# Optimization experiments

Hardware: AMD Instinct MI355X
Metric: run time of the kernel (lower is better)

Reference implementation:

```python
import jax, jax.numpy as jnp
import numpy as np

HID = 256
IN_DIM = 64
OUT_DIM = 4
B = 2048
T = 128


def setup_inputs() -> dict:
    key = jax.random.key(0)
    ks = jax.random.split(key, 12)
    s = lambda k, shp, fan: jax.random.normal(k, shp, jnp.float32) / np.sqrt(fan)
    return {
        "static_input": jax.random.normal(ks[0], (B, IN_DIM), jnp.float32),
        "times": jnp.arange(T, dtype=jnp.float32) * 0.05,  # increasing grid
        "W_in": s(ks[1], (IN_DIM, HID), IN_DIM), "b_in": jnp.zeros((HID,), jnp.float32),
        "W1": s(ks[2], (HID, HID), HID), "b1": jnp.zeros((HID,), jnp.float32),
        "W2": s(ks[3], (HID, HID), HID), "b2": jnp.zeros((HID,), jnp.float32),
        "W_pk": s(ks[4], (HID, OUT_DIM), HID), "b_pk": jnp.zeros((OUT_DIM,), jnp.float32),
        "W_pd": s(ks[5], (HID, 1), HID), "b_pd": jnp.zeros((1,), jnp.float32),
    }


def _odefunc(h, W1, b1, W2, b2):
    # Linear -> Tanh -> Linear (autonomous: ignores t, as in the torch ODEFunc)
    return jnp.tanh(h @ W1 + b1) @ W2 + b2


def reference(static_input, times, W_in, b_in, W1, b1, W2, b2, W_pk, b_pk, W_pd, b_pd):
    h0 = static_input @ W_in + b_in  # [B, H]
    f = lambda h: _odefunc(h, W1, b1, W2, b2)
    dts = times[1:] - times[:-1]  # [T-1]

    def rk4_step(h, dt):
        k1 = f(h)
        k2 = f(h + 0.5 * dt * k1)
        k3 = f(h + 0.5 * dt * k2)
        k4 = f(h + dt * k3)
        h_next = h + (dt / 6.0) * (k1 + 2.0 * k2 + 2.0 * k3 + k4)
        return h_next, h_next

    _, h_rest = jax.lax.scan(rk4_step, h0, dts)  # [T-1, B, H]
    h_ts = jnp.concatenate([h0[None], h_rest], axis=0)  # [T, B, H]
    h_ts = jnp.transpose(h_ts, (1, 0, 2))  # [B, T, H]
    pk_pred = h_ts @ W_pk + b_pk          # [B, T, OUT_DIM]
    pd_pred = h_ts[:, -1, :] @ W_pd + b_pd  # [B, 1]
    return (pk_pred, pd_pred)
```

## Files before the change

### kernel.cpp

```cpp
#include <hip/hip_runtime.h>
#include <hip/hip_bf16.h>
#include <stdint.h>

#define H       256
#define INDIM   64
#define TSTEPS  128
#define BATCH   2048
#define MROWS   8
#define OUTD    4

typedef __attribute__((ext_vector_type(8))) short bf16x8;
typedef __attribute__((ext_vector_type(4))) float f32x4;

__device__ __forceinline__ short b2s(float x) {
  __hip_bfloat16 h = __float2bfloat16(x);
  return __builtin_bit_cast(short, h);
}

__device__ __forceinline__ int swz(int m, int n) {
  return (m * H + n) ^ ((m & 7) << 3);
}

__device__ __forceinline__ float swap_hilo(float a, float b) {
#if __has_builtin(__builtin_amdgcn_permlane32_swap)
  typedef unsigned int u32x2 __attribute__((ext_vector_type(2)));
  u32x2 r = __builtin_amdgcn_permlane32_swap(
      __builtin_bit_cast(unsigned int, a),
      __builtin_bit_cast(unsigned int, b), false, false);
  return __builtin_bit_cast(float, r[0]);
#else
  float t = __shfl_xor(b, 32);
  return (threadIdx.x & 32) ? t : a;
#endif
}

__global__ __launch_bounds__(512, 1) void node_kernel(
    const float* __restrict__ g_static, const float* __restrict__ g_times,
    const float* __restrict__ g_Win, const float* __restrict__ g_bin,
    const float* __restrict__ g_W1, const float* __restrict__ g_b1,
    const float* __restrict__ g_W2, const float* __restrict__ g_b2,
    const float* __restrict__ g_Wpk, const float* __restrict__ g_bpk,
    const float* __restrict__ g_Wpd, const float* __restrict__ g_bpd,
    float* __restrict__ g_out)
{
  __shared__ __align__(16) short arg_lds[MROWS * H];
  __shared__ __align__(16) short h1_lds[MROWS * H];
  __shared__ __align__(16) short wpk_lds[8 * 64 * 8];
  __shared__ float h_lds[MROWS * H];
  __shared__ float s_lds[MROWS * INDIM];
  __shared__ float t_lds[TSTEPS];

  const int tid   = threadIdx.x;
  const int lane  = tid & 63;
  const int wid   = tid >> 6;
  const int g     = lane >> 4;
  const int c     = lane & 15;
  const int b0    = blockIdx.x * MROWS;
  const int ncol0 = wid * 32;
  const int am    = lane & 7;
  const int gg    = (lane >> 4) & 1;
  const int hh    = lane >> 5;
  const int colu  = ncol0 + 16 * hh + c;
  const int dm    = 4 * g;

  if (tid < TSTEPS) t_lds[tid] = g_times[tid];

  const float b1u2 = 2.0f * g_b1[colu];
  const float b2u  = g_b2[colu];
  const float bpkc = g_bpk[c & 3];
  const float bpdv = g_bpd[0];
  float wpd[4];
#pragma unroll
  for (int j = 0; j < 4; ++j) wpd[j] = g_Wpd[lane + 64 * j];

  int ra[8], wa[4], ha[4];
#pragma unroll
  for (int kt = 0; kt < 8; ++kt) ra[kt] = swz(am, kt * 32 + g * 8);
#pragma unroll
  for (int r = 0; r < 4; ++r) {
    wa[r] = swz(4 * gg + r, colu);
    ha[r] = (4 * gg + r) * H + colu;
  }

  bf16x8 w1f[8][2], w2f[8][2];
#pragma unroll
  for (int kt = 0; kt < 8; ++kt) {
#pragma unroll
    for (int nt = 0; nt < 2; ++nt) {
      const int n  = ncol0 + nt * 16 + c;
      const int kb = kt * 32 + g * 8;
      bf16x8 f1, f2;
#pragma unroll
      for (int u = 0; u < 8; ++u) {
        f1[u] = b2s(g_W1[(kb + u) * H + n]);
        f2[u] = b2s(g_W2[(kb + u) * H + n]);
      }
      w1f[kt][nt] = f1;
      w2f[kt][nt] = f2;
    }
  }

  if (wid == 0) {
#pragma unroll
    for (int kt = 0; kt < 8; ++kt) {
      bf16x8 f;
#pragma unroll
      for (int u = 0; u < 8; ++u) {
        const int k = kt * 32 + g * 8 + u;
        f[u] = (c < OUTD) ? b2s(g_Wpk[k * OUTD + c]) : (short)0;
      }
      *(bf16x8*)(wpk_lds + kt * 512 + lane * 8) = f;
    }
  }

  s_lds[tid] = g_static[(b0 + (tid >> 6)) * INDIM + (tid & 63)];
  __syncthreads();
  {
    const int m  = tid >> 6;
    const int n0 = (tid & 63) * 4;
    float a0 = g_bin[n0], a1 = g_bin[n0 + 1], a2 = g_bin[n0 + 2], a3 = g_bin[n0 + 3];
#pragma unroll 8
    for (int k = 0; k < INDIM; ++k) {
      const float sv = s_lds[m * INDIM + k];
      const f32x4 w = *(const f32x4*)(g_Win + k * H + n0);
      a0 += sv * w[0]; a1 += sv * w[1]; a2 += sv * w[2]; a3 += sv * w[3];
    }
    h_lds[m * H + n0] = a0;     h_lds[m * H + n0 + 1] = a1;
    h_lds[m * H + n0 + 2] = a2; h_lds[m * H + n0 + 3] = a3;
    arg_lds[swz(m, n0)]     = b2s(a0);
    arg_lds[swz(m, n0 + 1)] = b2s(a1);
    arg_lds[swz(m, n0 + 2)] = b2s(a2);
    arg_lds[swz(m, n0 + 3)] = b2s(a3);
  }
  __syncthreads();

  float hb[4];
#pragma unroll
  for (int r = 0; r < 4; ++r) hb[r] = h_lds[ha[r]];

  auto emit_pk = [&](int t) {
    if (wid == 0) {
      f32x4 acc = {0.f, 0.f, 0.f, 0.f};
#pragma unroll
      for (int kt = 0; kt < 8; ++kt) {
        const bf16x8 aA = *(const bf16x8*)(arg_lds + ra[kt]);
        const bf16x8 bW = *(const bf16x8*)(wpk_lds + kt * 512 + lane * 8);
        acc = __builtin_amdgcn_mfma_f32_16x16x32_bf16(aA, bW, acc, 0, 0, 0);
      }
      if (g < 2 && c < OUTD) {
#pragma unroll
        for (int r = 0; r < 4; ++r)
          g_out[((size_t)(b0 + dm + r) * TSTEPS + t) * OUTD + c] = acc[r] + bpkc;
      }
    }
  };

  emit_pk(0);

  for (int t = 1; t < TSTEPS; ++t) {
    const float dt = t_lds[t] - t_lds[t - 1];
    const float s6 = dt * (1.0f / 6.0f);
    float ks[4];

#pragma unroll
    for (int ev = 0; ev < 4; ++ev) {
      f32x4 A0 = {0.f,0.f,0.f,0.f}, A1 = {0.f,0.f,0.f,0.f};
      f32x4 B0 = {0.f,0.f,0.f,0.f}, B1 = {0.f,0.f,0.f,0.f};
#pragma unroll
      for (int kt = 0; kt < 4; ++kt) {
        const bf16x8 aA = *(const bf16x8*)(arg_lds + ra[kt]);
        const bf16x8 aB = *(const bf16x8*)(arg_lds + ra[kt + 4]);
        A0 = __builtin_amdgcn_mfma_f32_16x16x32_bf16(aA, w1f[kt][0], A0, 0, 0, 0);
        A1 = __builtin_amdgcn_mfma_f32_16x16x32_bf16(aA, w1f[kt][1], A1, 0, 0, 0);
        B0 = __builtin_amdgcn_mfma_f32_16x16x32_bf16(aB, w1f[kt + 4][0], B0, 0, 0, 0);
        B1 = __builtin_amdgcn_mfma_f32_16x16x32_bf16(aB, w1f[kt + 4][1], B1, 0, 0, 0);
      }
#pragma unroll
      for (int r = 0; r < 4; ++r) {
        const float v = swap_hilo(A0[r] + B0[r], A1[r] + B1[r]);
        const float e = __expf(__builtin_fmaf(2.0f, v, b1u2));
        const float th = 1.0f - __fdividef(2.0f, e + 1.0f);
        h1_lds[wa[r]] = b2s(th);
      }
      __syncthreads();

      A0 = f32x4{0.f,0.f,0.f,0.f}; A1 = f32x4{0.f,0.f,0.f,0.f};
      B0 = f32x4{0.f,0.f,0.f,0.f}; B1 = f32x4{0.f,0.f,0.f,0.f};
#pragma unroll
      for (int kt = 0; kt < 4; ++kt) {
        const bf16x8 aA = *(const bf16x8*)(h1_lds + ra[kt]);
        const bf16x8 aB = *(const bf16x8*)(h1_lds + ra[kt + 4]);
        A0 = __builtin_amdgcn_mfma_f32_16x16x32_bf16(aA, w2f[kt][0], A0, 0, 0, 0);
        A1 = __builtin_amdgcn_mfma_f32_16x16x32_bf16(aA, w2f[kt][1], A1, 0, 0, 0);
        B0 = __builtin_amdgcn_mfma_f32_16x16x32_bf16(aB, w2f[kt + 4][0], B0, 0, 0, 0);
        B1 = __builtin_amdgcn_mfma_f32_16x16x32_bf16(aB, w2f[kt + 4][1], B1, 0, 0, 0);
      }
#pragma unroll
      for (int r = 0; r < 4; ++r) {
        const float kv = swap_hilo(A0[r] + B0[r], A1[r] + B1[r]) + b2u;
        if (ev == 0)      ks[r] = kv;
        else if (ev == 3) ks[r] += kv;
        else              ks[r] += 2.0f * kv;
        if (ev < 3) {
          const float cc = (ev == 2) ? dt : 0.5f * dt;
          arg_lds[wa[r]] = b2s(__builtin_fmaf(cc, kv, hb[r]));
        } else {
          hb[r] = __builtin_fmaf(s6, ks[r], hb[r]);
          arg_lds[wa[r]] = b2s(hb[r]);
        }
      }
      __syncthreads();
    }
    emit_pk(t);
  }

#pragma unroll
  for (int r = 0; r < 4; ++r) h_lds[ha[r]] = hb[r];
  __syncthreads();
  {
    float p = 0.0f;
#pragma unroll
    for (int j = 0; j < 4; ++j) p += h_lds[wid * H + lane + 64 * j] * wpd[j];
#pragma unroll
    for (int m = 1; m < 64; m <<= 1) p += __shfl_xor(p, m);
    if (lane == 0) g_out[(size_t)BATCH * TSTEPS * OUTD + b0 + wid] = p + bpdv;
  }
}

extern "C" void kernel_launch(void* const* d_in, const int* in_sizes, int n_in,
                              void* d_out, int out_size, void* d_ws, size_t ws_size,
                              hipStream_t stream) {
  const float* g_static = (const float*)d_in[0];
  const float* g_times  = (const float*)d_in[1];
  const float* g_Win    = (const float*)d_in[2];
  const float* g_bin    = (const float*)d_in[3];
  const float* g_W1     = (const float*)d_in[4];
  const float* g_b1     = (const float*)d_in[5];
  const float* g_W2     = (const float*)d_in[6];
  const float* g_b2     = (const float*)d_in[7];
  const float* g_Wpk    = (const float*)d_in[8];
  const float* g_bpk    = (const float*)d_in[9];
  const float* g_Wpd    = (const float*)d_in[10];
  const float* g_bpd    = (const float*)d_in[11];

  node_kernel<<<dim3(BATCH / MROWS), dim3(512), 0, stream>>>(
      g_static, g_times, g_Win, g_bin, g_W1, g_b1, g_W2, g_b2,
      g_Wpk, g_bpk, g_Wpd, g_bpd, (float*)d_out);
}
```

Before: 660.7 us.

## Use 16-row batch tiles with 16 waves each owning 16 columns

Doubles the batch rows per block to 16 so each MFMA's 16 M-rows are all real work instead of half padding, and doubles threads to 1024 so each wave owns 16 hidden columns. Each wave's weight fragment register footprint halves and the permlane swap merge step goes away. The grid halves to 128 blocks, and every sync now involves 16 waves, which may hurt latency across the sequential RK4 chain. The Wpk LDS layout is also remapped so all 16 output rows come out correctly.

```diff
diff --git a/kernel.cpp b/kernel.cpp
--- a/kernel.cpp
+++ b/kernel.cpp
@@ -6,7 +6,7 @@
 #define INDIM   64
 #define TSTEPS  128
 #define BATCH   2048
-#define MROWS   8
+#define MROWS   16
 #define OUTD    4
 
 typedef __attribute__((ext_vector_type(8))) short bf16x8;
@@ -17,24 +17,17 @@
   return __builtin_bit_cast(short, h);
 }
 
-__device__ __forceinline__ int swz(int m, int n) {
-  return (m * H + n) ^ ((m & 7) << 3);
-}
-
-__device__ __forceinline__ float swap_hilo(float a, float b) {
-#if __has_builtin(__builtin_amdgcn_permlane32_swap)
-  typedef unsigned int u32x2 __attribute__((ext_vector_type(2)));
-  u32x2 r = __builtin_amdgcn_permlane32_swap(
-      __builtin_bit_cast(unsigned int, a),
-      __builtin_bit_cast(unsigned int, b), false, false);
-  return __builtin_bit_cast(float, r[0]);
-#else
-  float t = __shfl_xor(b, 32);
-  return (threadIdx.x & 32) ? t : a;
-#endif
-}
-
-__global__ __launch_bounds__(512, 1) void node_kernel(
+__device__ __forceinline__ int sidx(int m, int n) {
+  return m * H + (n ^ ((m & 7) << 3));
+}
+__device__ __forceinline__ int wpk_slot(int lane) {
+  return (((lane & 3) << 1) | ((lane >> 4) & 1)) |
+         (((lane >> 2) & 3) << 3) | (((lane >> 5) & 1) << 5);
+}
+
+#define MFMA(a, b, c) __builtin_amdgcn_mfma_f32_16x16x32_bf16((a), (b), (c), 0, 0, 0)
+
+__global__ __launch_bounds__(1024, 4) void node_kernel(
     const float* __restrict__ g_static, const float* __restrict__ g_times,
     const float* __restrict__ g_Win, const float* __restrict__ g_bin,
     const float* __restrict__ g_W1, const float* __restrict__ g_b1,
@@ -53,15 +46,12 @@
   const int tid   = threadIdx.x;
   const int lane  = tid & 63;
   const int wid   = tid >> 6;
-  const int g     = lane >> 4;
+  const int q     = lane >> 4;
   const int c     = lane & 15;
   const int b0    = blockIdx.x * MROWS;
-  const int ncol0 = wid * 32;
-  const int am    = lane & 7;
-  const int gg    = (lane >> 4) & 1;
-  const int hh    = lane >> 5;
-  const int colu  = ncol0 + 16 * hh + c;
-  const int dm    = 4 * g;
+  const int ncol0 = wid * 16;
+  const int arow  = lane & 15;
+  const int colu  = ncol0 + c;
 
   if (tid < TSTEPS) t_lds[tid] = g_times[tid];
 
@@ -75,49 +65,46 @@
 
   int ra[8], wa[4], ha[4];
 #pragma unroll
-  for (int kt = 0; kt < 8; ++kt) ra[kt] = swz(am, kt * 32 + g * 8);
+  for (int kt = 0; kt < 8; ++kt) ra[kt] = sidx(arow, kt * 32 + q * 8);
 #pragma unroll
   for (int r = 0; r < 4; ++r) {
-    wa[r] = swz(4 * gg + r, colu);
-    ha[r] = (4 * gg + r) * H + colu;
-  }
-
-  bf16x8 w1f[8][2], w2f[8][2];
+    wa[r] = sidx(4 * q + r, colu);
+    ha[r] = (4 * q + r) * H + colu;
+  }
+
+  bf16x8 w1f[8], w2f[8];
 #pragma unroll
   for (int kt = 0; kt < 8; ++kt) {
-#pragma unroll
-    for (int nt = 0; nt < 2; ++nt) {
-      const int n  = ncol0 + nt * 16 + c;
-      const int kb = kt * 32 + g * 8;
-      bf16x8 f1, f2;
-#pragma unroll
-      for (int u = 0; u < 8; ++u) {
-        f1[u] = b2s(g_W1[(kb + u) * H + n]);
-        f2[u] = b2s(g_W2[(kb + u) * H + n]);
-      }
-      w1f[kt][nt] = f1;
-      w2f[kt][nt] = f2;
-    }
+    const int kb = kt * 32 + q * 8;
+    bf16x8 f1, f2;
+#pragma unroll
+    for (int u = 0; u < 8; ++u) {
+      f1[u] = b2s(g_W1[(kb + u) * H + colu]);
+      f2[u] = b2s(g_W2[(kb + u) * H + colu]);
+    }
+    w1f[kt] = f1;
+    w2f[kt] = f2;
   }
 
   if (wid == 0) {
+    const int slot = wpk_slot(lane);
 #pragma unroll
     for (int kt = 0; kt < 8; ++kt) {
       bf16x8 f;
 #pragma unroll
       for (int u = 0; u < 8; ++u) {
-        const int k = kt * 32 + g * 8 + u;
+        const int k = kt * 32 + q * 8 + u;
         f[u] = (c < OUTD) ? b2s(g_Wpk[k * OUTD + c]) : (short)0;
       }
-      *(bf16x8*)(wpk_lds + kt * 512 + lane * 8) = f;
-    }
-  }
-
-  s_lds[tid] = g_static[(b0 + (tid >> 6)) * INDIM + (tid & 63)];
+      *(bf16x8*)(wpk_lds + kt * 512 + slot * 8) = f;
+    }
+  }
+
+  s_lds[tid] = g_static[(b0 + wid) * INDIM + lane];
   __syncthreads();
   {
-    const int m  = tid >> 6;
-    const int n0 = (tid & 63) * 4;
+    const int m  = wid;
+    const int n0 = lane * 4;
     float a0 = g_bin[n0], a1 = g_bin[n0 + 1], a2 = g_bin[n0 + 2], a3 = g_bin[n0 + 3];
 #pragma unroll 8
     for (int k = 0; k < INDIM; ++k) {
@@ -127,10 +114,10 @@
     }
     h_lds[m * H + n0] = a0;     h_lds[m * H + n0 + 1] = a1;
     h_lds[m * H + n0 + 2] = a2; h_lds[m * H + n0 + 3] = a3;
-    arg_lds[swz(m, n0)]     = b2s(a0);
-    arg_lds[swz(m, n0 + 1)] = b2s(a1);
-    arg_lds[swz(m, n0 + 2)] = b2s(a2);
-    arg_lds[swz(m, n0 + 3)] = b2s(a3);
+    arg_lds[sidx(m, n0)]     = b2s(a0);
+    arg_lds[sidx(m, n0 + 1)] = b2s(a1);
+    arg_lds[sidx(m, n0 + 2)] = b2s(a2);
+    arg_lds[sidx(m, n0 + 3)] = b2s(a3);
   }
   __syncthreads();
 
@@ -138,25 +125,27 @@
 #pragma unroll
   for (int r = 0; r < 4; ++r) hb[r] = h_lds[ha[r]];
 
+  const int wslot = wpk_slot(lane);
   auto emit_pk = [&](int t) {
     if (wid == 0) {
       f32x4 acc = {0.f, 0.f, 0.f, 0.f};
 #pragma unroll
       for (int kt = 0; kt < 8; ++kt) {
         const bf16x8 aA = *(const bf16x8*)(arg_lds + ra[kt]);
-        const bf16x8 bW = *(const bf16x8*)(wpk_lds + kt * 512 + lane * 8);
-        acc = __builtin_amdgcn_mfma_f32_16x16x32_bf16(aA, bW, acc, 0, 0, 0);
-      }
-      if (g < 2 && c < OUTD) {
+        const bf16x8 bW = *(const bf16x8*)(wpk_lds + kt * 512 + wslot * 8);
+        acc = MFMA(aA, bW, acc);
+      }
+      if (c < OUTD) {
 #pragma unroll
         for (int r = 0; r < 4; ++r)
-          g_out[((size_t)(b0 + dm + r) * TSTEPS + t) * OUTD + c] = acc[r] + bpkc;
+          g_out[((size_t)(b0 + 4 * q + r) * TSTEPS + t) * OUTD + c] = acc[r] + bpkc;
       }
     }
   };
 
   emit_pk(0);
 
+  const f32x4 vz = {0.f, 0.f, 0.f, 0.f};
   for (int t = 1; t < TSTEPS; ++t) {
     const float dt = t_lds[t] - t_lds[t - 1];
     const float s6 = dt * (1.0f / 6.0f);
@@ -164,49 +153,47 @@
 
 #pragma unroll
     for (int ev = 0; ev < 4; ++ev) {
-      f32x4 A0 = {0.f,0.f,0.f,0.f}, A1 = {0.f,0.f,0.f,0.f};
-      f32x4 B0 = {0.f,0.f,0.f,0.f}, B1 = {0.f,0.f,0.f,0.f};
-#pragma unroll
-      for (int kt = 0; kt < 4; ++kt) {
-        const bf16x8 aA = *(const bf16x8*)(arg_lds + ra[kt]);
-        const bf16x8 aB = *(const bf16x8*)(arg_lds + ra[kt + 4]);
-        A0 = __builtin_amdgcn_mfma_f32_16x16x32_bf16(aA, w1f[kt][0], A0, 0, 0, 0);
-        A1 = __builtin_amdgcn_mfma_f32_16x16x32_bf16(aA, w1f[kt][1], A1, 0, 0, 0);
-        B0 = __builtin_amdgcn_mfma_f32_16x16x32_bf16(aB, w1f[kt + 4][0], B0, 0, 0, 0);
-        B1 = __builtin_amdgcn_mfma_f32_16x16x32_bf16(aB, w1f[kt + 4][1], B1, 0, 0, 0);
-      }
-#pragma unroll
-      for (int r = 0; r < 4; ++r) {
-        const float v = swap_hilo(A0[r] + B0[r], A1[r] + B1[r]);
-        const float e = __expf(__builtin_fmaf(2.0f, v, b1u2));
-        const float th = 1.0f - __fdividef(2.0f, e + 1.0f);
-        h1_lds[wa[r]] = b2s(th);
+      {
+        f32x4 A0 = vz, B0 = vz;
+#pragma unroll
+        for (int i = 0; i < 4; ++i) {
+          const bf16x8 fA = *(const bf16x8*)(arg_lds + ra[i]);
+          const bf16x8 fB = *(const bf16x8*)(arg_lds + ra[i + 4]);
+          A0 = MFMA(fA, w1f[i], A0);
+          B0 = MFMA(fB, w1f[i + 4], B0);
+        }
+#pragma unroll
+        for (int r = 0; r < 4; ++r) {
+          const float v  = A0[r] + B0[r];
+          const float e  = __expf(__builtin_fmaf(2.0f, v, b1u2));
+          const float th = 1.0f - __fdividef(2.0f, e + 1.0f);
+          h1_lds[wa[r]] = b2s(th);
+        }
       }
       __syncthreads();
 
-      A0 = f32x4{0.f,0.f,0.f,0.f}; A1 = f32x4{0.f,0.f,0.f,0.f};
-      B0 = f32x4{0.f,0.f,0.f,0.f}; B1 = f32x4{0.f,0.f,0.f,0.f};
-#pragma unroll
-      for (int kt = 0; kt < 4; ++kt) {
-        const bf16x8 aA = *(const bf16x8*)(h1_lds + ra[kt]);
-        const bf16x8 aB = *(const bf16x8*)(h1_lds + ra[kt + 4]);
-        A0 = __builtin_amdgcn_mfma_f32_16x16x32_bf16(aA, w2f[kt][0], A0, 0, 0, 0);
-        A1 = __builtin_amdgcn_mfma_f32_16x16x32_bf16(aA, w2f[kt][1], A1, 0, 0, 0);
-        B0 = __builtin_amdgcn_mfma_f32_16x16x32_bf16(aB, w2f[kt + 4][0], B0, 0, 0, 0);
-        B1 = __builtin_amdgcn_mfma_f32_16x16x32_bf16(aB, w2f[kt + 4][1], B1, 0, 0, 0);
-      }
-#pragma unroll
-      for (int r = 0; r < 4; ++r) {
-        const float kv = swap_hilo(A0[r] + B0[r], A1[r] + B1[r]) + b2u;
-        if (ev == 0)      ks[r] = kv;
-        else if (ev == 3) ks[r] += kv;
-        else              ks[r] += 2.0f * kv;
-        if (ev < 3) {
-          const float cc = (ev == 2) ? dt : 0.5f * dt;
-          arg_lds[wa[r]] = b2s(__builtin_fmaf(cc, kv, hb[r]));
-        } else {
-          hb[r] = __builtin_fmaf(s6, ks[r], hb[r]);
-          arg_lds[wa[r]] = b2s(hb[r]);
+      {
+        f32x4 A0 = vz, B0 = vz;
+#pragma unroll
+        for (int i = 0; i < 4; ++i) {
+          const bf16x8 fA = *(const bf16x8*)(h1_lds + ra[i]);
+          const bf16x8 fB = *(const bf16x8*)(h1_lds + ra[i + 4]);
+          A0 = MFMA(fA, w2f[i], A0);
+          B0 = MFMA(fB, w2f[i + 4], B0);
+        }
+#pragma unroll
+        for (int r = 0; r < 4; ++r) {
+          const float kv = A0[r] + B0[r] + b2u;
+          if (ev == 0)      ks[r] = kv;
+          else if (ev == 3) ks[r] += kv;
+          else              ks[r] += 2.0f * kv;
+          if (ev < 3) {
+            const float cc = (ev == 2) ? dt : 0.5f * dt;
+            arg_lds[wa[r]] = b2s(__builtin_fmaf(cc, kv, hb[r]));
+          } else {
+            hb[r] = __builtin_fmaf(s6, ks[r], hb[r]);
+            arg_lds[wa[r]] = b2s(hb[r]);
+          }
         }
       }
       __syncthreads();
@@ -243,7 +230,7 @@
   const float* g_Wpd    = (const float*)d_in[10];
   const float* g_bpd    = (const float*)d_in[11];
 
-  node_kernel<<<dim3(BATCH / MROWS), dim3(512), 0, stream>>>(
+  node_kernel<<<dim3(BATCH / MROWS), dim3(1024), 0, stream>>>(
       g_static, g_times, g_Win, g_bin, g_W1, g_b1, g_W2, g_b2,
       g_Wpk, g_bpk, g_Wpd, g_bpd, (float*)d_out);
 }
```

Result: slower. 946.7 us (+43.3%).
